# Performance work log

Measured on AMD Instinct MI355X. Metric: run time of the kernel, lower is better.

## Reference

```python
import jax, jax.numpy as jnp
import numpy as np

CUTOFF = 3  # cutoff_freq default in low_pass_filter


def _low_pass(x):
    # full 2D FFT over (H, W), keep only the 4 corner blocks of size CUTOFF
    H, W = x.shape[-2], x.shape[-1]
    f = jnp.fft.fftn(x, axes=(-2, -1))
    mask = jnp.zeros((H, W), dtype=x.dtype)
    c = CUTOFF
    mask = mask.at[:c, :c].set(1).at[:c, -c:].set(1).at[-c:, :c].set(1).at[-c:, -c:].set(1)
    return jnp.abs(jnp.fft.ifftn(f * mask, axes=(-2, -1)))


def setup_inputs() -> dict:
    key = jax.random.key(0)
    k_x, k_w1, k_b1, k_w2, k_b2 = jax.random.split(key, 5)
    n_feat = 8
    B, C, H, W = 32, 3, 512, 512
    x = jax.random.uniform(k_x, (B, C, H, W), dtype=jnp.float32)
    # 1x1 convs == channel-mixing matrices; kaiming-ish scale
    w1 = jax.random.normal(k_w1, (n_feat, C), dtype=jnp.float32) * (1.0 / np.sqrt(C))
    b1 = jax.random.normal(k_b1, (n_feat,), dtype=jnp.float32) * 0.01
    w2 = jax.random.normal(k_w2, (C, n_feat), dtype=jnp.float32) * (1.0 / np.sqrt(n_feat))
    b2 = jax.random.normal(k_b2, (C,), dtype=jnp.float32) * 0.01
    return {"x": x, "w1": w1, "b1": b1, "w2": w2, "b2": b2}


def reference(x, w1, b1, w2, b2):
    lp = _low_pass(x)                                        # [B,3,H,W]
    h = jax.nn.relu(jnp.einsum('bchw,fc->bfhw', lp, w1) + b1[None, :, None, None])
    y = jnp.einsum('bfhw,cf->bchw', h, w2) + b2[None, :, None, None]
    return jnp.clip(y + lp, 0.0, 1.0)
```

## Files before the change

kernel.cpp:

```cpp
#include <hip/hip_runtime.h>
#include <math.h>


#define WS_TS 0
#define WS_F  6144
#define WS_A  12288
constexpr int NPART = 8;

#define CJ0 1.0f
#define CJ1 0.99992470183914450299f
#define CJ2 0.99969881869620422012f
#define CJ3 0.99932238458834954375f
#define CJ4 0.99879545620517239271f
#define CJ5 0.99811811290014917919f
#define CJ6 0.99729045667869021614f
#define CJ7 0.99631261218277800129f
#define SJ0 0.0f
#define SJ1 0.01227153828571992539f
#define SJ2 0.02454122852291228803f
#define SJ3 0.03680722294135883171f
#define SJ4 0.04906767432741801425f
#define SJ5 0.06132073630220857829f
#define SJ6 0.07356456359966742631f
#define SJ7 0.08579731234443989385f

__global__ __launch_bounds__(256, 6) void k_colsum(const float* __restrict__ x,
                                                   float* __restrict__ ws) {
    __shared__ float buf[3][64][15];
    float* A = ws + WS_A;
    int img = blockIdx.x >> 5;
    int sub = blockIdx.x & 31;
    int stripe = sub & 3;
    int hgrp = sub >> 2;
    int t = threadIdx.x;
    int wave = t >> 6;
    int lane = t & 63;
    int w = stripe * 128 + lane * 2;
    int H = hgrp * 32 + wave * 8;
    const float* xp = x + (size_t)img * 262144 + (size_t)H * 512 + w;

    const float TH = 6.28318530717958647692f / 512.0f;
    float pc1, ps1, pc2, ps2, pc3, ps3;
    sincosf(TH * (float)H, &ps1, &pc1);
    pc2 = pc1 * pc1 - ps1 * ps1;  ps2 = 2.f * pc1 * ps1;
    pc3 = pc1 * pc2 - ps1 * ps2;  ps3 = ps1 * pc2 + pc1 * ps2;

    float s0[2] = {0, 0};
    float ar1[2] = {0, 0}, ai1[2] = {0, 0};
    float ar2[2] = {0, 0}, ai2[2] = {0, 0};
    float ar3[2] = {0, 0}, ai3[2] = {0, 0};

#define ROW(J, CJ, SJ)                                                        \
    {                                                                         \
        float2 xa = *(const float2*)(xp + (size_t)(J) * 512);                 \
        float2 xb = *(const float2*)(xp + (size_t)((J) * 512 + 131072));      \
        float u0 = xa.x + xb.x, u1 = xa.y + xb.y;                             \
        float v0 = xa.x - xb.x, v1 = xa.y - xb.y;                             \
        float cj1 = pc1 * (CJ) - ps1 * (SJ);                                  \
        float sj1 = ps1 * (CJ) + pc1 * (SJ);                                  \
        float cj2 = cj1 * cj1 - sj1 * sj1;                                    \
        float sj2 = 2.f * cj1 * sj1;                                          \
        float cj3 = cj1 * cj2 - sj1 * sj2;                                    \
        float sj3 = sj1 * cj2 + cj1 * sj2;                                    \
        s0[0] += u0;               s0[1] += u1;                               \
        ar1[0] = fmaf(v0, cj1, ar1[0]);  ai1[0] = fmaf(-v0, sj1, ai1[0]);     \
        ar1[1] = fmaf(v1, cj1, ar1[1]);  ai1[1] = fmaf(-v1, sj1, ai1[1]);     \
        ar2[0] = fmaf(u0, cj2, ar2[0]);  ai2[0] = fmaf(-u0, sj2, ai2[0]);     \
        ar2[1] = fmaf(u1, cj2, ar2[1]);  ai2[1] = fmaf(-u1, sj2, ai2[1]);     \
        ar3[0] = fmaf(v0, cj3, ar3[0]);  ai3[0] = fmaf(-v0, sj3, ai3[0]);     \
        ar3[1] = fmaf(v1, cj3, ar3[1]);  ai3[1] = fmaf(-v1, sj3, ai3[1]);     \
    }

    ROW(0, CJ0, SJ0)
    ROW(1, CJ1, SJ1)
    ROW(2, CJ2, SJ2)
    ROW(3, CJ3, SJ3)
    ROW(4, CJ4, SJ4)
    ROW(5, CJ5, SJ5)
    ROW(6, CJ6, SJ6)
    ROW(7, CJ7, SJ7)
#undef ROW

    if (wave != 0) {
        float* r = &buf[wave - 1][lane][0];
        r[0] = s0[0];   r[1] = s0[1];
        r[2] = ar1[0];  r[3] = ar1[1];  r[4] = ai1[0];  r[5] = ai1[1];
        r[6] = ar2[0];  r[7] = ar2[1];  r[8] = ai2[0];  r[9] = ai2[1];
        r[10] = ar3[0]; r[11] = ar3[1]; r[12] = ai3[0]; r[13] = ai3[1];
    }
    __syncthreads();
    if (wave == 0) {
#pragma unroll
        for (int v = 0; v < 3; ++v) {
            const float* r = &buf[v][lane][0];
            s0[0] += r[0];   s0[1] += r[1];
            ar1[0] += r[2];  ar1[1] += r[3];  ai1[0] += r[4];  ai1[1] += r[5];
            ar2[0] += r[6];  ar2[1] += r[7];  ai2[0] += r[8];  ai2[1] += r[9];
            ar3[0] += r[10]; ar3[1] += r[11]; ai3[0] += r[12]; ai3[1] += r[13];
        }
        float* Ab = A + (((size_t)img * NPART + hgrp) * 8) * 512 + w;
        *(float2*)(Ab + 0 * 512) = make_float2(s0[0], s0[1]);
        *(float2*)(Ab + 1 * 512) = make_float2(0.f, 0.f);
        *(float2*)(Ab + 2 * 512) = make_float2(ar1[0], ar1[1]);
        *(float2*)(Ab + 3 * 512) = make_float2(ai1[0], ai1[1]);
        *(float2*)(Ab + 4 * 512) = make_float2(ar2[0], ar2[1]);
        *(float2*)(Ab + 5 * 512) = make_float2(ai2[0], ai2[1]);
        *(float2*)(Ab + 6 * 512) = make_float2(ar3[0], ar3[1]);
        *(float2*)(Ab + 7 * 512) = make_float2(ai3[0], ai3[1]);
    }
}

__global__ __launch_bounds__(256) void k_proj(float* __restrict__ ws) {
    int t = threadIdx.x;
    if (blockIdx.x == 96) {
        const float STEP = 6.28318530717958647692f / 512.0f;
        const int mv[6] = {0, 1, 2, -3, -2, -1};
        for (int h = t; h < 512; h += 256) {
            float* tsp = ws + WS_TS + h * 12;
#pragma unroll
            for (int i = 0; i < 6; ++i) {
                int r = ((mv[i] * h) % 512 + 512) & 511;
                float s, c;
                sincosf(STEP * (float)r, &s, &c);
                tsp[2 * i] = c; tsp[2 * i + 1] = s;
            }
        }
        return;
    }
    __shared__ float As[8][8][68];
    __shared__ float Rs[28][8][2];
    const float* A = ws + WS_A;
    float* F = ws + WS_F;
    int img = blockIdx.x;

    {
        int plane = t >> 5;
        int w0 = (t & 31) * 16;
        float4 acc[4];
#pragma unroll
        for (int u = 0; u < 4; ++u) acc[u] = make_float4(0.f, 0.f, 0.f, 0.f);
        const float* base = A + ((size_t)img * NPART * 8 + plane) * 512 + w0;
        for (int hg = 0; hg < NPART; ++hg) {
            const float* p = base + (size_t)hg * 8 * 512;
#pragma unroll
            for (int u = 0; u < 4; ++u) {
                float4 v = *(const float4*)(p + u * 4);
                acc[u].x += v.x; acc[u].y += v.y; acc[u].z += v.z; acc[u].w += v.w;
            }
        }
        int seg = w0 >> 6, j0 = w0 & 63;
#pragma unroll
        for (int u = 0; u < 4; ++u)
            *(float4*)&As[plane][seg][j0 + u * 4] = acc[u];
    }
    __syncthreads();

    if (t < 224) {
        int pair = t >> 3, seg = t & 7;
        int k = pair / 7, mi = pair % 7;
        float m = (float)(mi - 3);
        const float TH = 6.28318530717958647692f / 512.0f;
        float cm, sm, pc, ps;
        sincosf(-m * TH, &sm, &cm);
        sincosf(-m * TH * (float)(seg * 64), &ps, &pc);
        const float* Ar_ = &As[2 * k][seg][0];
        const float* Ai_ = &As[2 * k + 1][seg][0];
        float pre = 0.f, pim = 0.f;
#pragma unroll 4
        for (int j = 0; j < 64; ++j) {
            float Ar = Ar_[j], Ai = Ai_[j];
            pre += Ar * pc - Ai * ps;
            pim += Ar * ps + Ai * pc;
            float n = pc * cm - ps * sm;
            ps = ps * cm + pc * sm;
            pc = n;
        }
        Rs[pair][seg][0] = pre;
        Rs[pair][seg][1] = pim;
    }
    __syncthreads();
    if (t < 56) {
        int pair = t >> 1, part = t & 1;
        float s = 0.f;
#pragma unroll
        for (int g = 0; g < 8; ++g) s += Rs[pair][g][part];
        F[(size_t)img * 56 + t] = s;
    }
}

__global__ __launch_bounds__(256) void k_out(const float* __restrict__ ws,
                                             const float* __restrict__ w1,
                                             const float* __restrict__ b1,
                                             const float* __restrict__ w2,
                                             const float* __restrict__ b2,
                                             float* __restrict__ out) {
    const float* tabS = ws + WS_TS;
    const float* Fb = ws + WS_F;
    __shared__ float F_lds[3][56];
    __shared__ float T[4][3][12];
    int t = threadIdx.x;
    int blk = blockIdx.x;
    int b = blk >> 7;
    int h0 = (blk & 127) << 2;

    if (t < 168) {
        int c = t / 56, comp = t % 56;
        F_lds[c][comp] = Fb[(size_t)(b * 3 + c) * 56 + comp];
    }

    float rw1[8][3], rb1[8], rw2[3][8], rb2[3];
#pragma unroll
    for (int f_ = 0; f_ < 8; ++f_) {
        rb1[f_] = b1[f_];
#pragma unroll
        for (int c = 0; c < 3; ++c) rw1[f_][c] = w1[f_ * 3 + c];
    }
#pragma unroll
    for (int c = 0; c < 3; ++c) {
        rb2[c] = b2[c];
#pragma unroll
        for (int f_ = 0; f_ < 8; ++f_) rw2[c][f_] = w2[c * 8 + f_];
    }
    __syncthreads();

    if (t < 72) {
        int rl = t / 18, rem = t % 18;
        int c = rem / 6, kc = rem % 6;
        int h = h0 + rl;
        const float* th = tabS + h * 12;
        int m_kc = (kc < 3) ? kc : kc - 6;
        const float inv = 1.0f / (512.0f * 512.0f);
        float tre = 0.f, tim = 0.f;
#pragma unroll
        for (int kr = 0; kr < 6; ++kr) {
            int kk, mi; float csign;
            if (kr < 3) { kk = kr;     mi = m_kc + 3; csign =  1.f; }
            else        { kk = 6 - kr; mi = 3 - m_kc; csign = -1.f; }
            int pair = kk * 7 + mi;
            float fr = F_lds[c][pair * 2] * inv;
            float fi = F_lds[c][pair * 2 + 1] * csign * inv;
            float cc = th[kr * 2], ss = th[kr * 2 + 1];
            tre += fr * cc - fi * ss;
            tim += fr * ss + fi * cc;
        }
        T[rl][c][kc * 2]     = tre;
        T[rl][c][kc * 2 + 1] = tim;
    }
    __syncthreads();

    int rl = t >> 6, lane = t & 63;
    int h = h0 + rl;
    float A0r[3], A0i[3], U1r[3], U1i[3], V1r[3], V1i[3];
    float U2r[3], U2i[3], V2r[3], V2i[3], Br[3], Bi[3];
#pragma unroll
    for (int c = 0; c < 3; ++c) {
        const float* Tc = T[rl][c];
        A0r[c] = Tc[0];  A0i[c] = Tc[1];
        float t1r = Tc[2],  t1i = Tc[3];
        float t2r = Tc[4],  t2i = Tc[5];
        float bmr = Tc[6],  bmi = Tc[7];
        float m2r = Tc[8],  m2i = Tc[9];
        float m1r = Tc[10], m1i = Tc[11];
        U1r[c] = t1r + m1r; U1i[c] = t1i + m1i;
        V1r[c] = t1r - m1r; V1i[c] = t1i - m1i;
        U2r[c] = t2r + m2r; U2i[c] = t2i + m2i;
        V2r[c] = t2r - m2r; V2i[c] = t2i - m2i;
        Br[c] = bmr; Bi[c] = bmi;
    }
    const float* tw = tabS + lane * 12;
    float c1 = tw[2], s1 = tw[3];
    float c2 = tw[4], s2 = tw[5];
    float c3 = tw[6], s3 = -tw[7];
    const float K = 0.70710678118654752440f;
    float* ob = out + ((size_t)(b * 3) * 512 + h) * 512;

#pragma unroll
    for (int j = 0; j < 8; ++j) {
        int w = lane + 64 * j;
        float lp[3];
#pragma unroll
        for (int c = 0; c < 3; ++c) {
            float re = A0r[c] + U1r[c] * c1 - V1i[c] * s1
                              + U2r[c] * c2 - V2i[c] * s2
                              + Br[c] * c3 + Bi[c] * s3;
            float im = A0i[c] + U1i[c] * c1 + V1r[c] * s1
                              + U2i[c] * c2 + V2r[c] * s2
                              + Bi[c] * c3 - Br[c] * s3;
            lp[c] = sqrtf(re * re + im * im);
        }
        float hid[8];
#pragma unroll
        for (int f_ = 0; f_ < 8; ++f_) {
            float v = rb1[f_] + lp[0] * rw1[f_][0] + lp[1] * rw1[f_][1] + lp[2] * rw1[f_][2];
            hid[f_] = fmaxf(v, 0.0f);
        }
#pragma unroll
        for (int c = 0; c < 3; ++c) {
            float y = rb2[c] + lp[c];
#pragma unroll
            for (int f_ = 0; f_ < 8; ++f_) y += hid[f_] * rw2[c][f_];
            y = fminf(fmaxf(y, 0.0f), 1.0f);
            ob[(size_t)c * 262144 + w] = y;
        }
        if (j < 7) {
            float nc1 = K * (c1 - s1), ns1 = K * (c1 + s1);
            float nc2 = -s2,           ns2 = c2;
            float nc3 = -K * (c3 + s3), ns3 = K * (c3 - s3);
            c1 = nc1; s1 = ns1; c2 = nc2; s2 = ns2; c3 = nc3; s3 = ns3;
        }
    }
}

extern "C" void kernel_launch(void* const* d_in, const int* in_sizes, int n_in,
                              void* d_out, int out_size, void* d_ws, size_t ws_size,
                              hipStream_t stream) {
    const float* x  = (const float*)d_in[0];
    const float* w1 = (const float*)d_in[1];
    const float* b1 = (const float*)d_in[2];
    const float* w2 = (const float*)d_in[3];
    const float* b2 = (const float*)d_in[4];
    float* out = (float*)d_out;
    float* ws = (float*)d_ws;

    hipLaunchKernelGGL(k_colsum, dim3(96 * 32), dim3(256), 0, stream, x, ws);
    hipLaunchKernelGGL(k_proj, dim3(97), dim3(256), 0, stream, ws);
    hipLaunchKernelGGL(k_out, dim3(4096), dim3(256), 0, stream, ws, w1, b1, w2, b2, out);
}
```

Measured before the change: 66.51 us.

## Fuse three kernels into one cooperative persistent kernel with grid syncs

Replaces the three back-to-back launches (column sums, projection, output) with a single cooperative persistent kernel. Blocks loop over work units and separate the phases with grid.sync, and the original three-kernel path is kept as a fallback if the cooperative launch fails. The aim is to remove inter-kernel launch gaps and tail drain. In exchange it caps occupancy at a fixed grid, adds grid-wide barrier cost, adds extra __syncthreads per unit, and runs an occupancy query on the host each call.

```diff
diff --git a/kernel.cpp b/kernel.cpp
--- a/kernel.cpp
+++ b/kernel.cpp
@@ -1,5 +1,8 @@
 #include <hip/hip_runtime.h>
+#include <hip/hip_cooperative_groups.h>
 #include <math.h>
+
+namespace cg = cooperative_groups;
 
 
 #define WS_TS 0
@@ -24,22 +27,22 @@
 #define SJ6 0.07356456359966742631f
 #define SJ7 0.08579731234443989385f
 
-__global__ __launch_bounds__(256, 6) void k_colsum(const float* __restrict__ x,
-                                                   float* __restrict__ ws) {
-    __shared__ float buf[3][64][15];
-    float* A = ws + WS_A;
-    int img = blockIdx.x >> 5;
-    int sub = blockIdx.x & 31;
+
+__device__ __forceinline__ void phaseA_unit(const float* __restrict__ x,
+                                            float* __restrict__ A,
+                                            float* __restrict__ smem,
+                                            int unit, int t) {
+    float (*buf)[64][15] = (float (*)[64][15])smem;
+    const float TH = 6.28318530717958647692f / 512.0f;
+    int wave = t >> 6, lane = t & 63;
+    int img = unit >> 5;
+    int sub = unit & 31;
     int stripe = sub & 3;
     int hgrp = sub >> 2;
-    int t = threadIdx.x;
-    int wave = t >> 6;
-    int lane = t & 63;
     int w = stripe * 128 + lane * 2;
     int H = hgrp * 32 + wave * 8;
     const float* xp = x + (size_t)img * 262144 + (size_t)H * 512 + w;
 
-    const float TH = 6.28318530717958647692f / 512.0f;
     float pc1, ps1, pc2, ps2, pc3, ps3;
     sincosf(TH * (float)H, &ps1, &pc1);
     pc2 = pc1 * pc1 - ps1 * ps1;  ps2 = 2.f * pc1 * ps1;
@@ -70,7 +73,6 @@
         ar3[0] = fmaf(v0, cj3, ar3[0]);  ai3[0] = fmaf(-v0, sj3, ai3[0]);     \
         ar3[1] = fmaf(v1, cj3, ar3[1]);  ai3[1] = fmaf(-v1, sj3, ai3[1]);     \
     }
-
     ROW(0, CJ0, SJ0)
     ROW(1, CJ1, SJ1)
     ROW(2, CJ2, SJ2)
@@ -108,31 +110,31 @@
         *(float2*)(Ab + 6 * 512) = make_float2(ar3[0], ar3[1]);
         *(float2*)(Ab + 7 * 512) = make_float2(ai3[0], ai3[1]);
     }
-}
-
-__global__ __launch_bounds__(256) void k_proj(float* __restrict__ ws) {
-    int t = threadIdx.x;
-    if (blockIdx.x == 96) {
-        const float STEP = 6.28318530717958647692f / 512.0f;
-        const int mv[6] = {0, 1, 2, -3, -2, -1};
-        for (int h = t; h < 512; h += 256) {
-            float* tsp = ws + WS_TS + h * 12;
-#pragma unroll
-            for (int i = 0; i < 6; ++i) {
-                int r = ((mv[i] * h) % 512 + 512) & 511;
-                float s, c;
-                sincosf(STEP * (float)r, &s, &c);
-                tsp[2 * i] = c; tsp[2 * i + 1] = s;
-            }
-        }
-        return;
-    }
-    __shared__ float As[8][8][68];
-    __shared__ float Rs[28][8][2];
-    const float* A = ws + WS_A;
-    float* F = ws + WS_F;
-    int img = blockIdx.x;
-
+    __syncthreads();
+}
+
+__device__ __forceinline__ void phaseB_table(float* __restrict__ ws, int t) {
+    const float TH = 6.28318530717958647692f / 512.0f;
+    const int mv[6] = {0, 1, 2, -3, -2, -1};
+    for (int h = t; h < 512; h += 256) {
+        float* tsp = ws + WS_TS + h * 12;
+#pragma unroll
+        for (int i = 0; i < 6; ++i) {
+            int r = ((mv[i] * h) % 512 + 512) & 511;
+            float s, c;
+            sincosf(TH * (float)r, &s, &c);
+            tsp[2 * i] = c; tsp[2 * i + 1] = s;
+        }
+    }
+}
+
+__device__ __forceinline__ void phaseB_proj(const float* __restrict__ A,
+                                            float* __restrict__ F,
+                                            float* __restrict__ smem,
+                                            int img, int t) {
+    float (*As)[8][68] = (float (*)[8][68])smem;
+    float (*Rs)[8][2] = (float (*)[8][2])(smem + 4352);
+    const float TH = 6.28318530717958647692f / 512.0f;
     {
         int plane = t >> 5;
         int w0 = (t & 31) * 16;
@@ -154,12 +156,10 @@
             *(float4*)&As[plane][seg][j0 + u * 4] = acc[u];
     }
     __syncthreads();
-
     if (t < 224) {
         int pair = t >> 3, seg = t & 7;
         int k = pair / 7, mi = pair % 7;
         float m = (float)(mi - 3);
-        const float TH = 6.28318530717958647692f / 512.0f;
         float cm, sm, pc, ps;
         sincosf(-m * TH, &sm, &cm);
         sincosf(-m * TH * (float)(seg * 64), &ps, &pc);
@@ -186,43 +186,27 @@
         for (int g = 0; g < 8; ++g) s += Rs[pair][g][part];
         F[(size_t)img * 56 + t] = s;
     }
-}
-
-__global__ __launch_bounds__(256) void k_out(const float* __restrict__ ws,
-                                             const float* __restrict__ w1,
-                                             const float* __restrict__ b1,
-                                             const float* __restrict__ w2,
-                                             const float* __restrict__ b2,
-                                             float* __restrict__ out) {
+    __syncthreads();
+}
+
+__device__ __forceinline__ void phaseC_tile(const float* __restrict__ ws,
+                                            const float rw1[8][3], const float rb1[8],
+                                            const float rw2[3][8], const float rb2[3],
+                                            float* __restrict__ out,
+                                            float* __restrict__ smem,
+                                            int tile, int t) {
     const float* tabS = ws + WS_TS;
     const float* Fb = ws + WS_F;
-    __shared__ float F_lds[3][56];
-    __shared__ float T[4][3][12];
-    int t = threadIdx.x;
-    int blk = blockIdx.x;
-    int b = blk >> 7;
-    int h0 = (blk & 127) << 2;
-
+    float (*F_lds)[56] = (float (*)[56])smem;
+    float (*T)[3][12] = (float (*)[3][12])(smem + 168);
+    int b = tile >> 7;
+    int h0 = (tile & 127) << 2;
+    __syncthreads();
     if (t < 168) {
         int c = t / 56, comp = t % 56;
         F_lds[c][comp] = Fb[(size_t)(b * 3 + c) * 56 + comp];
     }
-
-    float rw1[8][3], rb1[8], rw2[3][8], rb2[3];
-#pragma unroll
-    for (int f_ = 0; f_ < 8; ++f_) {
-        rb1[f_] = b1[f_];
-#pragma unroll
-        for (int c = 0; c < 3; ++c) rw1[f_][c] = w1[f_ * 3 + c];
-    }
-#pragma unroll
-    for (int c = 0; c < 3; ++c) {
-        rb2[c] = b2[c];
-#pragma unroll
-        for (int f_ = 0; f_ < 8; ++f_) rw2[c][f_] = w2[c * 8 + f_];
-    }
-    __syncthreads();
-
+    __syncthreads();
     if (t < 72) {
         int rl = t / 18, rem = t % 18;
         int c = rem / 6, kc = rem % 6;
@@ -311,6 +295,83 @@
     }
 }
 
+
+__global__ __launch_bounds__(256, 2) void k_fused(const float* __restrict__ x,
+                                                  const float* __restrict__ w1,
+                                                  const float* __restrict__ b1,
+                                                  const float* __restrict__ w2,
+                                                  const float* __restrict__ b2,
+                                                  float* __restrict__ out,
+                                                  float* __restrict__ ws) {
+    cg::grid_group grid = cg::this_grid();
+    __shared__ float smem[4800];
+    int t = threadIdx.x;
+    int bid = blockIdx.x;
+    int nblk = gridDim.x;
+    float* A = ws + WS_A;
+
+    for (int unit = bid; unit < 3072; unit += nblk)
+        phaseA_unit(x, A, smem, unit, t);
+    grid.sync();
+
+    if (bid == 96) phaseB_table(ws, t);
+    else if (bid < 96) phaseB_proj(A, ws + WS_F, smem, bid, t);
+    grid.sync();
+
+    float rw1[8][3], rb1[8], rw2[3][8], rb2[3];
+#pragma unroll
+    for (int f_ = 0; f_ < 8; ++f_) {
+        rb1[f_] = b1[f_];
+#pragma unroll
+        for (int c = 0; c < 3; ++c) rw1[f_][c] = w1[f_ * 3 + c];
+    }
+#pragma unroll
+    for (int c = 0; c < 3; ++c) {
+        rb2[c] = b2[c];
+#pragma unroll
+        for (int f_ = 0; f_ < 8; ++f_) rw2[c][f_] = w2[c * 8 + f_];
+    }
+    for (int tile = bid; tile < 4096; tile += nblk)
+        phaseC_tile(ws, rw1, rb1, rw2, rb2, out, smem, tile, t);
+}
+
+
+__global__ __launch_bounds__(256, 6) void k_colsum(const float* __restrict__ x,
+                                                   float* __restrict__ ws) {
+    __shared__ float smem[2880];
+    phaseA_unit(x, ws + WS_A, smem, blockIdx.x, threadIdx.x);
+}
+
+__global__ __launch_bounds__(256) void k_proj(float* __restrict__ ws) {
+    __shared__ float smem[4800];
+    if (blockIdx.x == 96) { phaseB_table(ws, threadIdx.x); return; }
+    phaseB_proj(ws + WS_A, ws + WS_F, smem, blockIdx.x, threadIdx.x);
+}
+
+__global__ __launch_bounds__(256) void k_out(const float* __restrict__ ws,
+                                             const float* __restrict__ w1,
+                                             const float* __restrict__ b1,
+                                             const float* __restrict__ w2,
+                                             const float* __restrict__ b2,
+                                             float* __restrict__ out) {
+    __shared__ float smem[320];
+    int t = threadIdx.x;
+    float rw1[8][3], rb1[8], rw2[3][8], rb2[3];
+#pragma unroll
+    for (int f_ = 0; f_ < 8; ++f_) {
+        rb1[f_] = b1[f_];
+#pragma unroll
+        for (int c = 0; c < 3; ++c) rw1[f_][c] = w1[f_ * 3 + c];
+    }
+#pragma unroll
+    for (int c = 0; c < 3; ++c) {
+        rb2[c] = b2[c];
+#pragma unroll
+        for (int f_ = 0; f_ < 8; ++f_) rw2[c][f_] = w2[c * 8 + f_];
+    }
+    phaseC_tile(ws, rw1, rb1, rw2, rb2, out, smem, blockIdx.x, t);
+}
+
 extern "C" void kernel_launch(void* const* d_in, const int* in_sizes, int n_in,
                               void* d_out, int out_size, void* d_ws, size_t ws_size,
                               hipStream_t stream) {
@@ -322,7 +383,28 @@
     float* out = (float*)d_out;
     float* ws = (float*)d_ws;
 
-    hipLaunchKernelGGL(k_colsum, dim3(96 * 32), dim3(256), 0, stream, x, ws);
-    hipLaunchKernelGGL(k_proj, dim3(97), dim3(256), 0, stream, ws);
-    hipLaunchKernelGGL(k_out, dim3(4096), dim3(256), 0, stream, ws, w1, b1, w2, b2, out);
-}
+    bool coop_done = false;
+    int maxActive = 0;
+    if (hipOccupancyMaxActiveBlocksPerMultiprocessor(
+            &maxActive, (const void*)k_fused, 256, 0) == hipSuccess &&
+        maxActive >= 1) {
+        int nblk = maxActive * 256;
+        if (nblk > 1024) nblk = 1024;
+        void* args[] = {(void*)&x, (void*)&w1, (void*)&b1, (void*)&w2,
+                        (void*)&b2, (void*)&out, (void*)&ws};
+        hipError_t e = hipLaunchCooperativeKernel((const void*)k_fused,
+                                                  dim3(nblk), dim3(256),
+                                                  args, 0, stream);
+        if (e == hipSuccess) coop_done = true;
+        else (void)hipGetLastError();
+    } else {
+        (void)hipGetLastError();
+    }
+
+    if (!coop_done) {
+        hipLaunchKernelGGL(k_colsum, dim3(96 * 32), dim3(256), 0, stream, x, ws);
+        hipLaunchKernelGGL(k_proj, dim3(97), dim3(256), 0, stream, ws);
+        hipLaunchKernelGGL(k_out, dim3(4096), dim3(256), 0, stream,
+                           ws, w1, b1, w2, b2, out);
+    }
+}
```

Result: slower. 193.9 us (+191.5%).
